# Kernel optimization log

Measured on AMD Instinct MI355X. Metric: run time of the kernel, lower is better.

## Reference

```python
import jax, jax.numpy as jnp
import numpy as np
from jax import lax

NUM_HEADS = 4
EPS = 1e-12  # torch F.normalize eps


def _dwconv3(x, w):
    # depthwise 3x3 conv, padding 1; w: (C,1,3,3)
    return lax.conv_general_dilated(
        x, w, window_strides=(1, 1), padding=((1, 1), (1, 1)),
        dimension_numbers=('NCHW', 'OIHW', 'NCHW'),
        feature_group_count=w.shape[0])


def _make_qkv(x, w_qkv, w_dw):
    # 1x1 conv (GEMM over channels) then depthwise 3x3
    y = jnp.einsum('bchw,oc->bohw', x, w_qkv)
    y = _dwconv3(y, w_dw)
    b, c3, h, w = y.shape
    c = c3 // 3
    q, k, v = jnp.split(y, 3, axis=1)
    rs = lambda t: t.reshape(b, NUM_HEADS, c // NUM_HEADS, h * w)
    return rs(q), rs(k), rs(v)


def _l2norm(t):
    # F.normalize(t, dim=-1): t / max(||t||_2, eps)
    n = jnp.sqrt(jnp.sum(t * t, axis=-1, keepdims=True))
    return t / jnp.maximum(n, EPS)


def _attend(q, k, v, temperature):
    # channel-wise attention: scores are (b, h, d, d)
    scores = jnp.einsum('bhdn,bhen->bhde', q, k) * temperature
    attn = jax.nn.softmax(scores, axis=-1)
    return jnp.einsum('bhde,bhen->bhdn', attn, v), attn


def setup_inputs() -> dict:
    key = jax.random.key(0)
    ks = jax.random.split(key, 8)
    B, C, H, W = 4, 192, 128, 128
    C3 = 3 * C
    return {
        'e': jax.random.normal(ks[0], (B, C, H, W), jnp.float32),
        'd': jax.random.normal(ks[1], (B, C, H, W), jnp.float32),
        'temperature': jnp.ones((1, NUM_HEADS, 1, 1), jnp.float32),
        'w_qkv': jax.random.normal(ks[2], (C3, C), jnp.float32) * 0.05,
        'w_dw': jax.random.normal(ks[3], (C3, 1, 3, 3), jnp.float32) * 0.1,
        'w_p1': jax.random.normal(ks[4], (C, C), jnp.float32) * 0.05,
        'w_p2': jax.random.normal(ks[5], (C, C), jnp.float32) * 0.05,
        'w_p3': jax.random.normal(ks[6], (C, C), jnp.float32) * 0.05,
        'w_p4': jax.random.normal(ks[7], (C, C), jnp.float32) * 0.05,
    }


def reference(e, d, temperature, w_qkv, w_dw, w_p1, w_p2, w_p3, w_p4):
    b, c, h, w = e.shape
    q_e, k_e, v_e = _make_qkv(e, w_qkv, w_dw)
    q_d, k_d, v_d = _make_qkv(d, w_qkv, w_dw)
    q_e, k_e = _l2norm(q_e), _l2norm(k_e)
    q_d, k_d = _l2norm(q_d), _l2norm(k_d)

    proj = lambda o, wp: jnp.einsum('bchw,oc->bohw', o.reshape(b, c, h, w), wp)

    out_ee, _ = _attend(q_e, k_e, v_e, temperature)
    out_dd, _ = _attend(q_d, k_d, v_d, temperature)
    intra_e = proj(out_ee, w_p1)
    intra_d = proj(out_dd, w_p2)

    out_ed, _ = _attend(q_e, k_d, v_d, temperature)
    # cross d->e: replicate torch's squeeze(0) (no-op unless b==1)
    scores_de = jnp.einsum('bhdn,bhen->bhde', q_d, k_e) * temperature
    attn_de = jax.nn.softmax(scores_de, axis=-1)
    if attn_de.shape[0] == 1:
        attn_de = attn_de[0]
    out_de = jnp.einsum('...de,bhen->bhdn', attn_de, v_e)
    inter_ed = proj(out_ed, w_p3)
    inter_de = proj(out_de, w_p4)
    return (intra_e, intra_d, inter_ed, inter_de)
```

## Files before the change

kernel.cpp:

```cpp
#include <hip/hip_runtime.h>

#define N_PIX 16384
#define CC 192
#define C3 576
#define KTOT 192
#define NCH 32
#define CHUNK 512

typedef __bf16 bf16_t;
typedef bf16_t bf16x4 __attribute__((ext_vector_type(4)));
typedef bf16_t bf16x8 __attribute__((ext_vector_type(8)));
typedef float f32x4 __attribute__((ext_vector_type(4)));

struct WPtrs { const float* p[4]; };
struct GArgs { const float* W[16]; long xoff[16]; long yoff[16]; int sel[16]; };

template <typename XT, typename YT, int NC, int NMT>
__global__ __launch_bounds__(256) void gemm_mloop(GArgs ga,
    const XT* __restrict__ X0, const XT* __restrict__ X1, YT* __restrict__ Y)
{
    __shared__ __align__(16) bf16_t Wl[64][200];
    const int z = blockIdx.y;
    const XT* __restrict__ Xb = (ga.sel[z] ? X1 : X0) + ga.xoff[z];
    const int n0 = blockIdx.x * 128;
    const int tid = threadIdx.x;
    const int w = tid >> 6;
    const int gi = (tid >> 4) & 3;
    const int li = tid & 15;

    bf16x8 xfrag[6][2];
    #pragma unroll
    for (int t = 0; t < 6; ++t)
        #pragma unroll
        for (int ni = 0; ni < 2; ++ni) {
            const XT* xp = Xb + (long)(32 * t + 8 * gi) * N_PIX
                              + n0 + 32 * w + 16 * ni + li;
            bf16x8 v;
            #pragma unroll
            for (int e = 0; e < 8; ++e) v[e] = (bf16_t)xp[(long)e * N_PIX];
            xfrag[t][ni] = v;
        }

    const int wr = tid >> 2, wkb = (tid & 3) * 48;
    float wreg[48];
    auto loadW = [&](int it) {
        const int c = it / NMT, j = it % NMT;
        const float* base = ga.W[z * NC + c] + (long)(64 * j + wr) * KTOT + wkb;
        #pragma unroll
        for (int q = 0; q < 12; ++q) {
            float4 a = *(const float4*)(base + 4 * q);
            wreg[4 * q + 0] = a.x; wreg[4 * q + 1] = a.y;
            wreg[4 * q + 2] = a.z; wreg[4 * q + 3] = a.w;
        }
    };
    auto writeW = [&]() {
        #pragma unroll
        for (int s = 0; s < 6; ++s) {
            bf16x8 v = { (bf16_t)wreg[8 * s + 0], (bf16_t)wreg[8 * s + 1],
                         (bf16_t)wreg[8 * s + 2], (bf16_t)wreg[8 * s + 3],
                         (bf16_t)wreg[8 * s + 4], (bf16_t)wreg[8 * s + 5],
                         (bf16_t)wreg[8 * s + 6], (bf16_t)wreg[8 * s + 7] };
            *(bf16x8*)&Wl[wr][wkb + 8 * s] = v;
        }
    };

    loadW(0);
    writeW();
    __syncthreads();

    for (int it = 0; it < NC * NMT; ++it) {
        if (it + 1 < NC * NMT) loadW(it + 1);
        f32x4 acc[4][2];
        #pragma unroll
        for (int i = 0; i < 4; ++i)
            #pragma unroll
            for (int j = 0; j < 2; ++j) acc[i][j] = 0.f;
        #pragma unroll
        for (int t = 0; t < 6; ++t) {
            bf16x8 af[4];
            #pragma unroll
            for (int mi = 0; mi < 4; ++mi)
                af[mi] = *(const bf16x8*)&Wl[16 * mi + li][32 * t + 8 * gi];
            #pragma unroll
            for (int mi = 0; mi < 4; ++mi)
                #pragma unroll
                for (int ni = 0; ni < 2; ++ni)
                    acc[mi][ni] = __builtin_amdgcn_mfma_f32_16x16x32_bf16(
                        af[mi], xfrag[t][ni], acc[mi][ni], 0, 0, 0);
        }
        {
            const int c = it / NMT, j = it % NMT;
            YT* Yb = Y + ga.yoff[z * NC + c] + (long)(64 * j) * N_PIX;
            #pragma unroll
            for (int mi = 0; mi < 4; ++mi)
                #pragma unroll
                for (int ni = 0; ni < 2; ++ni) {
                    const int n = n0 + 32 * w + 16 * ni + li;
                    #pragma unroll
                    for (int r = 0; r < 4; ++r)
                        Yb[(long)(16 * mi + 4 * gi + r) * N_PIX + n] =
                            (YT)acc[mi][ni][r];
                }
        }
        __syncthreads();
        if (it + 1 < NC * NMT) {
            writeW();
            __syncthreads();
        }
    }
}

__global__ __launch_bounds__(256) void dwconv3b(const bf16_t* __restrict__ Yin,
    const float* __restrict__ wdw, bf16_t* __restrict__ Z,
    float* __restrict__ invn)
{
    const int ch = blockIdx.x, sb = blockIdx.y;
    const int tid = threadIdx.x;
    const int x0 = (tid & 15) << 3;
    const int y0 = (tid >> 4) << 3;
    const bf16_t* __restrict__ inp = Yin + (long)(sb * C3 + ch) * N_PIX;
    bf16_t* __restrict__ outp = Z + (long)(sb * C3 + ch) * N_PIX;
    const float* wch = wdw + ch * 9;
    const float w00 = wch[0], w01 = wch[1], w02 = wch[2];
    const float w10 = wch[3], w11 = wch[4], w12 = wch[5];
    const float w20 = wch[6], w21 = wch[7], w22 = wch[8];
    const bool hasL = (x0 > 0), hasR = (x0 < 120);
    float A[10], B[10], Cr[10];
    auto loadrow = [&](int yy, float* r) {
        if (yy < 0 || yy > 127) {
            #pragma unroll
            for (int i = 0; i < 10; ++i) r[i] = 0.f;
            return;
        }
        const bf16_t* p = inp + (yy << 7);
        bf16x8 v = *(const bf16x8*)(p + x0);
        #pragma unroll
        for (int j = 0; j < 8; ++j) r[1 + j] = (float)v[j];
        r[0] = hasL ? (float)p[x0 - 1] : 0.f;
        r[9] = hasR ? (float)p[x0 + 8] : 0.f;
    };
    loadrow(y0 - 1, A);
    loadrow(y0,     B);
    float ss = 0.f;
    #pragma unroll
    for (int r = 0; r < 8; ++r) {
        loadrow(y0 + r + 1, Cr);
        bf16x8 ov;
        #pragma unroll
        for (int i = 0; i < 8; ++i) {
            float s;
            s = fmaf(w00, A[i],  fmaf(w01, A[i + 1],  w02 * A[i + 2]));
            s = fmaf(w10, B[i],  fmaf(w11, B[i + 1],  fmaf(w12, B[i + 2], s)));
            s = fmaf(w20, Cr[i], fmaf(w21, Cr[i + 1], fmaf(w22, Cr[i + 2], s)));
            ov[i] = (bf16_t)s;
            const float vb = (float)ov[i];
            ss = fmaf(vb, vb, ss);
        }
        *(bf16x8*)(outp + ((y0 + r) << 7) + x0) = ov;
        #pragma unroll
        for (int i = 0; i < 10; ++i) { A[i] = B[i]; B[i] = Cr[i]; }
    }
    if (ch < 384) {
        #pragma unroll
        for (int off = 32; off > 0; off >>= 1) ss += __shfl_down(ss, off);
        __shared__ float red[4];
        if ((tid & 63) == 0) red[tid >> 6] = ss;
        __syncthreads();
        if (tid == 0) {
            const float t = red[0] + red[1] + red[2] + red[3];
            const int row = (sb >> 2) * 1536 + (sb & 3) * 384 + ch;
            invn[row] = 1.f / fmaxf(sqrtf(t), 1e-12f);
        }
    }
}

__global__ __launch_bounds__(256) void scores_mfma(const bf16_t* __restrict__ Z,
                                                   float* __restrict__ part)
{
    const int c = blockIdx.x;
    const int bh = blockIdx.y;
    const int b = bh >> 2, h = bh & 3;
    __shared__ __align__(16) bf16_t T[4][48][72];
    const int tid = threadIdx.x;
    const int m = tid >> 6;
    const int gi = (tid >> 4) & 3, li = tid & 15;
    const int qs = (m == 1 || m == 3) ? 1 : 0;
    const int ks = (m == 1 || m == 2) ? 1 : 0;
    f32x4 acc[3][3];
    #pragma unroll
    for (int i = 0; i < 3; ++i)
        #pragma unroll
        for (int j = 0; j < 3; ++j) acc[i][j] = 0.f;

    const int nbase = c * CHUNK;
    for (int k0 = 0; k0 < CHUNK; k0 += 64) {
        __syncthreads();
        for (int l = tid; l < 1536; l += 256) {
            const int t = l / 384;
            const int rem = l - t * 384;
            const int r = rem >> 3, s = rem & 7;
            const int sidx = (t < 2) ? t : (t - 2);
            const int qk = (t < 2) ? 0 : 1;
            const bf16_t* gp = Z + ((long)((sidx * 4 + b) * C3 + qk * 192 + h * 48 + r)) * N_PIX
                                 + nbase + k0 + s * 8;
            *(bf16x8*)&T[t][r][s * 8] = *(const bf16x8*)gp;
        }
        __syncthreads();
        #pragma unroll
        for (int k2 = 0; k2 < 64; k2 += 32) {
            bf16x8 af[3], bfr[3];
            #pragma unroll
            for (int i = 0; i < 3; ++i) {
                bf16x4 lo = *(const bf16x4*)&T[qs][16 * i + li][k2 + 4 * gi];
                bf16x4 hi = *(const bf16x4*)&T[qs][16 * i + li][k2 + 16 + 4 * gi];
                af[i] = __builtin_shufflevector(lo, hi, 0, 1, 2, 3, 4, 5, 6, 7);
            }
            #pragma unroll
            for (int j = 0; j < 3; ++j) {
                bf16x4 lo = *(const bf16x4*)&T[2 + ks][16 * j + li][k2 + 4 * gi];
                bf16x4 hi = *(const bf16x4*)&T[2 + ks][16 * j + li][k2 + 16 + 4 * gi];
                bfr[j] = __builtin_shufflevector(lo, hi, 0, 1, 2, 3, 4, 5, 6, 7);
            }
            #pragma unroll
            for (int i = 0; i < 3; ++i)
                #pragma unroll
                for (int j = 0; j < 3; ++j)
                    acc[i][j] = __builtin_amdgcn_mfma_f32_16x16x32_bf16(
                        af[i], bfr[j], acc[i][j], 0, 0, 0);
        }
    }
    const long base = ((long)(m * 16 + bh) * NCH + c) * 2304;
    #pragma unroll
    for (int i = 0; i < 3; ++i)
        #pragma unroll
        for (int j = 0; j < 3; ++j) {
            const int e = 16 * j + li;
            #pragma unroll
            for (int r = 0; r < 4; ++r) {
                const int d = 16 * i + 4 * gi + r;
                part[base + d * 48 + e] = acc[i][j][r];
            }
        }
}

__global__ __launch_bounds__(256) void reduce_softmax(const float* __restrict__ part,
    const float* __restrict__ invn, const float* __restrict__ temp,
    float* __restrict__ attn)
{
    const int mbh = blockIdx.x;
    const int m = mbh >> 4, b = (mbh >> 2) & 3, h = mbh & 3;
    const int qs = (m == 1 || m == 3) ? 1 : 0;
    const int ks = (m == 1 || m == 2) ? 1 : 0;
    __shared__ float sm[48][48];
    const int tid = threadIdx.x;
    const long pbase = (long)mbh * NCH * 2304;
    const float T = temp[h];
    for (int idx = tid; idx < 2304; idx += 256) {
        float v = 0.f;
        #pragma unroll 8
        for (int c = 0; c < NCH; ++c) v += part[pbase + c * 2304 + idx];
        const int d = idx / 48, e = idx % 48;
        const float iq = invn[(qs * 4 + b) * 384 + h * 48 + d];
        const float ik = invn[(ks * 4 + b) * 384 + 192 + h * 48 + e];
        sm[d][e] = v * iq * ik * T;
    }
    __syncthreads();
    if (tid < 48) {
        float mx = -1e30f;
        #pragma unroll
        for (int e = 0; e < 48; ++e) mx = fmaxf(mx, sm[tid][e]);
        float sum = 0.f;
        #pragma unroll
        for (int e = 0; e < 48; ++e) {
            const float v = __expf(sm[tid][e] - mx);
            sm[tid][e] = v;
            sum += v;
        }
        const float inv = 1.f / sum;
        const long abase = (long)mbh * 2304 + (long)tid * 48;
        #pragma unroll
        for (int e = 0; e < 48; ++e) attn[abase + e] = sm[tid][e] * inv;
    }
}

__global__ __launch_bounds__(256) void make_M(const float* __restrict__ attn,
                                              WPtrs wp, float* __restrict__ M)
{
    const int h = blockIdx.x & 3;
    const int b = (blockIdx.x >> 2) & 3;
    const int m = blockIdx.x >> 4;
    __shared__ float A[48][48];
    const int tid = threadIdx.x;
    if (m == 3) {
        for (int l = tid; l < 2304; l += 256) {
            float s = 0.f;
            #pragma unroll
            for (int bb = 0; bb < 16; ++bb)
                s += attn[(long)(48 + bb) * 2304 + l];
            A[l / 48][l % 48] = s;
        }
    } else {
        const long ab = (long)(m * 16 + b * 4 + h) * 2304;
        for (int l = tid; l < 2304; l += 256)
            A[l / 48][l % 48] = attn[ab + l];
    }
    __syncthreads();
    const float* W = wp.p[m];
    float* Mo = M + (long)(m * 4 + b) * 192 * 192;
    for (int o = tid >> 4; o < 192; o += 16) {
        const float* wrow = W + (long)o * 192 + h * 48;
        for (int e2 = tid & 15; e2 < 48; e2 += 16) {
            float s = 0.f;
            #pragma unroll
            for (int d = 0; d < 48; ++d) s = fmaf(wrow[d], A[d][e2], s);
            Mo[(long)o * 192 + h * 48 + e2] = s;
        }
    }
}

extern "C" void kernel_launch(void* const* d_in, const int* in_sizes, int n_in,
                              void* d_out, int out_size, void* d_ws, size_t ws_size,
                              hipStream_t stream)
{
    const float* e     = (const float*)d_in[0];
    const float* d     = (const float*)d_in[1];
    const float* temp  = (const float*)d_in[2];
    const float* w_qkv = (const float*)d_in[3];
    const float* w_dw  = (const float*)d_in[4];
    const float* w_p1  = (const float*)d_in[5];
    const float* w_p2  = (const float*)d_in[6];
    const float* w_p3  = (const float*)d_in[7];
    const float* w_p4  = (const float*)d_in[8];
    float* out = (float*)d_out;
    float* ws  = (float*)d_ws;

    bf16_t* zraw = (bf16_t*)ws;
    bf16_t* zb   = (bf16_t*)(ws + 37748736L);
    float* attn  = ws + 75497472L;
    float* invn  = ws + 75644928L;
    float* part  = ws;
    float* Mmat  = ws + 8388608L;

    const long sXin = (long)CC * N_PIX;
    const long sQKV = (long)C3 * N_PIX;

    GArgs gq{};
    for (int z = 0; z < 8; ++z) {
        gq.W[z] = w_qkv;
        gq.xoff[z] = (long)(z & 3) * sXin;
        gq.yoff[z] = (long)z * sQKV;
        gq.sel[z] = z >> 2;
    }
    gemm_mloop<float, bf16_t, 1, 9><<<dim3(128, 8), 256, 0, stream>>>(gq, e, d, zraw);
    dwconv3b<<<dim3(C3, 8), 256, 0, stream>>>(zraw, w_dw, zb, invn);
    scores_mfma<<<dim3(NCH, 16), 256, 0, stream>>>(zb, part);
    reduce_softmax<<<dim3(64), 256, 0, stream>>>(part, invn, temp, attn);
    WPtrs wpj; wpj.p[0] = w_p1; wpj.p[1] = w_p2; wpj.p[2] = w_p3; wpj.p[3] = w_p4;
    make_M<<<dim3(64), 256, 0, stream>>>(attn, wpj, Mmat);
    GArgs gm{};
    for (int z = 0; z < 8; ++z) {
        const int s = z >> 2, b = z & 3;
        gm.xoff[z] = ((long)((s * 4 + b) * C3 + 384)) * N_PIX;
        gm.sel[z] = 0;
        for (int c = 0; c < 2; ++c) {
            const int midx = (s == 0) ? (c ? 3 : 0) : (c ? 2 : 1);
            gm.W[2 * z + c] = Mmat + (long)(midx * 4 + b) * 192 * 192;
            gm.yoff[2 * z + c] = (long)(midx * 4 + b) * sXin;
        }
    }
    gemm_mloop<bf16_t, float, 2, 3><<<dim3(128, 8), 256, 0, stream>>>(gm, zb, zb, out);
}
```

Baseline: 334.2 us.

## Pre-pad bf16 weight tiles and stream them into LDS via double-buffered DMA

Weights for both GEMMs are now converted once to bf16 in a padded tile layout: a new prep_w kernel does this for w_qkv, and make_M writes its output in the same format. The GEMM then copies each tile straight into double-buffered LDS with global_load_lds, replacing the register load, convert and LDS store, and dropping one barrier per iteration. The MFMA operands are swapped so each lane holds four consecutive pixels, which allows vectorized f32x4/bf16x4 output stores. The cost is an extra small kernel launch, more LDS per block, and correctness depends on the async LDS copies completing before the barrier.

```diff
diff --git a/kernel.cpp b/kernel.cpp
--- a/kernel.cpp
+++ b/kernel.cpp
@@ -6,6 +6,7 @@
 #define KTOT 192
 #define NCH 32
 #define CHUNK 512
+#define WTILE 12800
 
 typedef __bf16 bf16_t;
 typedef bf16_t bf16x4 __attribute__((ext_vector_type(4)));
@@ -13,13 +14,14 @@
 typedef float f32x4 __attribute__((ext_vector_type(4)));
 
 struct WPtrs { const float* p[4]; };
-struct GArgs { const float* W[16]; long xoff[16]; long yoff[16]; int sel[16]; };
+struct GArgs { long xoff[16]; long yoff[16]; long woff[16]; int sel[16]; };
 
 template <typename XT, typename YT, int NC, int NMT>
 __global__ __launch_bounds__(256) void gemm_mloop(GArgs ga,
-    const XT* __restrict__ X0, const XT* __restrict__ X1, YT* __restrict__ Y)
-{
-    __shared__ __align__(16) bf16_t Wl[64][200];
+    const XT* __restrict__ X0, const XT* __restrict__ X1,
+    YT* __restrict__ Y, const bf16_t* __restrict__ Wpad)
+{
+    __shared__ __align__(16) bf16_t Wl[2][WTILE];
     const int z = blockIdx.y;
     const XT* __restrict__ Xb = (ga.sel[z] ? X1 : X0) + ga.xoff[z];
     const int n0 = blockIdx.x * 128;
@@ -41,52 +43,51 @@
             xfrag[t][ni] = v;
         }
 
-    const int wr = tid >> 2, wkb = (tid & 3) * 48;
-    float wreg[48];
-    auto loadW = [&](int it) {
+    auto dmaW = [&](int it, int buf) {
         const int c = it / NMT, j = it % NMT;
-        const float* base = ga.W[z * NC + c] + (long)(64 * j + wr) * KTOT + wkb;
-        #pragma unroll
-        for (int q = 0; q < 12; ++q) {
-            float4 a = *(const float4*)(base + 4 * q);
-            wreg[4 * q + 0] = a.x; wreg[4 * q + 1] = a.y;
-            wreg[4 * q + 2] = a.z; wreg[4 * q + 3] = a.w;
-        }
+        const char* src = (const char*)(Wpad + ga.woff[z * NC + c]
+                                        + (long)j * WTILE);
+        char* dst = (char*)&Wl[buf][0];
+        #pragma unroll
+        for (int r = 0; r < 6; ++r)
+            __builtin_amdgcn_global_load_lds(
+                (const __attribute__((address_space(1))) void*)
+                    (src + r * 4096 + tid * 16),
+                (__attribute__((address_space(3))) void*)
+                    (dst + r * 4096 + w * 1024),
+                16, 0, 0);
+        if (w == 0)
+            __builtin_amdgcn_global_load_lds(
+                (const __attribute__((address_space(1))) void*)
+                    (src + 24576 + tid * 16),
+                (__attribute__((address_space(3))) void*)(dst + 24576),
+                16, 0, 0);
     };
-    auto writeW = [&]() {
-        #pragma unroll
-        for (int s = 0; s < 6; ++s) {
-            bf16x8 v = { (bf16_t)wreg[8 * s + 0], (bf16_t)wreg[8 * s + 1],
-                         (bf16_t)wreg[8 * s + 2], (bf16_t)wreg[8 * s + 3],
-                         (bf16_t)wreg[8 * s + 4], (bf16_t)wreg[8 * s + 5],
-                         (bf16_t)wreg[8 * s + 6], (bf16_t)wreg[8 * s + 7] };
-            *(bf16x8*)&Wl[wr][wkb + 8 * s] = v;
-        }
-    };
-
-    loadW(0);
-    writeW();
+
+    dmaW(0, 0);
     __syncthreads();
 
     for (int it = 0; it < NC * NMT; ++it) {
-        if (it + 1 < NC * NMT) loadW(it + 1);
+        const int cur = it & 1;
+        if (it + 1 < NC * NMT) dmaW(it + 1, cur ^ 1);
         f32x4 acc[4][2];
         #pragma unroll
         for (int i = 0; i < 4; ++i)
             #pragma unroll
-            for (int j = 0; j < 2; ++j) acc[i][j] = 0.f;
+            for (int jj = 0; jj < 2; ++jj) acc[i][jj] = 0.f;
         #pragma unroll
         for (int t = 0; t < 6; ++t) {
             bf16x8 af[4];
             #pragma unroll
             for (int mi = 0; mi < 4; ++mi)
-                af[mi] = *(const bf16x8*)&Wl[16 * mi + li][32 * t + 8 * gi];
+                af[mi] = *(const bf16x8*)
+                    &Wl[cur][(16 * mi + li) * 200 + 32 * t + 8 * gi];
             #pragma unroll
             for (int mi = 0; mi < 4; ++mi)
                 #pragma unroll
                 for (int ni = 0; ni < 2; ++ni)
                     acc[mi][ni] = __builtin_amdgcn_mfma_f32_16x16x32_bf16(
-                        af[mi], xfrag[t][ni], acc[mi][ni], 0, 0, 0);
+                        xfrag[t][ni], af[mi], acc[mi][ni], 0, 0, 0);
         }
         {
             const int c = it / NMT, j = it % NMT;
@@ -95,18 +96,31 @@
             for (int mi = 0; mi < 4; ++mi)
                 #pragma unroll
                 for (int ni = 0; ni < 2; ++ni) {
-                    const int n = n0 + 32 * w + 16 * ni + li;
-                    #pragma unroll
-                    for (int r = 0; r < 4; ++r)
-                        Yb[(long)(16 * mi + 4 * gi + r) * N_PIX + n] =
-                            (YT)acc[mi][ni][r];
+                    YT* yp = Yb + (long)(16 * mi + li) * N_PIX
+                               + n0 + 32 * w + 16 * ni + 4 * gi;
+                    if constexpr (sizeof(YT) == 4) {
+                        *(f32x4*)yp = acc[mi][ni];
+                    } else {
+                        bf16x4 v = { (bf16_t)acc[mi][ni][0],
+                                     (bf16_t)acc[mi][ni][1],
+                                     (bf16_t)acc[mi][ni][2],
+                                     (bf16_t)acc[mi][ni][3] };
+                        *(bf16x4*)yp = v;
+                    }
                 }
         }
         __syncthreads();
-        if (it + 1 < NC * NMT) {
-            writeW();
-            __syncthreads();
-        }
+    }
+}
+
+__global__ __launch_bounds__(256) void prep_w(const float* __restrict__ wq,
+                                              bf16_t* __restrict__ wpad)
+{
+    const int j = blockIdx.x, tid = threadIdx.x;
+    for (int idx = tid; idx < 64 * 192; idx += 256) {
+        const int r = idx / 192, c = idx - r * 192;
+        wpad[(long)j * WTILE + r * 200 + c] =
+            (bf16_t)wq[(long)(64 * j + r) * KTOT + c];
     }
 }
 
@@ -284,7 +298,7 @@
 }
 
 __global__ __launch_bounds__(256) void make_M(const float* __restrict__ attn,
-                                              WPtrs wp, float* __restrict__ M)
+                                              WPtrs wp, bf16_t* __restrict__ Mpad)
 {
     const int h = blockIdx.x & 3;
     const int b = (blockIdx.x >> 2) & 3;
@@ -306,14 +320,15 @@
     }
     __syncthreads();
     const float* W = wp.p[m];
-    float* Mo = M + (long)(m * 4 + b) * 192 * 192;
+    bf16_t* Mo = Mpad + (long)(m * 4 + b) * 3 * WTILE;
     for (int o = tid >> 4; o < 192; o += 16) {
         const float* wrow = W + (long)o * 192 + h * 48;
+        bf16_t* orow = Mo + (long)(o >> 6) * WTILE + (o & 63) * 200 + h * 48;
         for (int e2 = tid & 15; e2 < 48; e2 += 16) {
             float s = 0.f;
             #pragma unroll
             for (int d = 0; d < 48; ++d) s = fmaf(wrow[d], A[d][e2], s);
-            Mo[(long)o * 192 + h * 48 + e2] = s;
+            orow[e2] = (bf16_t)s;
         }
     }
 }
@@ -338,25 +353,28 @@
     bf16_t* zb   = (bf16_t*)(ws + 37748736L);
     float* attn  = ws + 75497472L;
     float* invn  = ws + 75644928L;
+    bf16_t* Wqpad = (bf16_t*)(ws + 75648000L);
+    bf16_t* Mpad  = (bf16_t*)(ws + 75710000L);
     float* part  = ws;
-    float* Mmat  = ws + 8388608L;
 
     const long sXin = (long)CC * N_PIX;
     const long sQKV = (long)C3 * N_PIX;
 
+    prep_w<<<dim3(9), 256, 0, stream>>>(w_qkv, Wqpad);
     GArgs gq{};
     for (int z = 0; z < 8; ++z) {
-        gq.W[z] = w_qkv;
         gq.xoff[z] = (long)(z & 3) * sXin;
         gq.yoff[z] = (long)z * sQKV;
+        gq.woff[z] = 0;
         gq.sel[z] = z >> 2;
     }
-    gemm_mloop<float, bf16_t, 1, 9><<<dim3(128, 8), 256, 0, stream>>>(gq, e, d, zraw);
+    gemm_mloop<float, bf16_t, 1, 9><<<dim3(128, 8), 256, 0, stream>>>(
+        gq, e, d, zraw, Wqpad);
     dwconv3b<<<dim3(C3, 8), 256, 0, stream>>>(zraw, w_dw, zb, invn);
     scores_mfma<<<dim3(NCH, 16), 256, 0, stream>>>(zb, part);
     reduce_softmax<<<dim3(64), 256, 0, stream>>>(part, invn, temp, attn);
     WPtrs wpj; wpj.p[0] = w_p1; wpj.p[1] = w_p2; wpj.p[2] = w_p3; wpj.p[3] = w_p4;
-    make_M<<<dim3(64), 256, 0, stream>>>(attn, wpj, Mmat);
+    make_M<<<dim3(64), 256, 0, stream>>>(attn, wpj, Mpad);
     GArgs gm{};
     for (int z = 0; z < 8; ++z) {
         const int s = z >> 2, b = z & 3;
@@ -364,9 +382,10 @@
         gm.sel[z] = 0;
         for (int c = 0; c < 2; ++c) {
             const int midx = (s == 0) ? (c ? 3 : 0) : (c ? 2 : 1);
-            gm.W[2 * z + c] = Mmat + (long)(midx * 4 + b) * 192 * 192;
+            gm.woff[2 * z + c] = (long)(midx * 4 + b) * 3 * WTILE;
             gm.yoff[2 * z + c] = (long)(midx * 4 + b) * sXin;
         }
     }
-    gemm_mloop<bf16_t, float, 2, 3><<<dim3(128, 8), 256, 0, stream>>>(gm, zb, zb, out);
-}
+    gemm_mloop<bf16_t, float, 2, 3><<<dim3(128, 8), 256, 0, stream>>>(
+        gm, zb, zb, out, Mpad);
+}
```

Result: no change. 339.1 us (+1.5%).
